# Performance work log

Measured on AMD Instinct MI355X. Metric: run time of the kernel, lower is better.

The kernel has to match this reference:

```python
import jax, jax.numpy as jnp
import numpy as np

B, N, F, NF = 4, 256, 256, 192
BN_EPS = 1e-5
NEG_SLOPE = 0.01  # torch F.leaky_relu default


def setup_inputs() -> dict:
    key = jax.random.key(0)
    ks = jax.random.split(key, 6)
    x = jax.random.normal(ks[0], (B, N, F), dtype=jnp.float32)
    # W_id is the identity adjacency broadcast to [B, N, N, 1]
    W_id = jnp.broadcast_to(jnp.eye(N, dtype=jnp.float32)[None, :, :, None], (B, N, N, 1))
    # conv2d_1: 1x1 conv, weight [nf, F, 1, 1] -> store as [F, nf]
    w1 = jax.random.normal(ks[1], (F, NF), dtype=jnp.float32) / np.sqrt(F)
    b1 = jax.random.normal(ks[2], (NF,), dtype=jnp.float32) * 0.01
    gamma = jnp.ones((NF,), dtype=jnp.float32)
    beta = jnp.zeros((NF,), dtype=jnp.float32)
    # conv2d_last: 1x1 conv nf -> 1
    w2 = jax.random.normal(ks[3], (NF,), dtype=jnp.float32) / np.sqrt(NF)
    b2 = jax.random.normal(ks[4], (), dtype=jnp.float32) * 0.01
    return {"x": x, "W_id": W_id, "w1": w1, "b1": b1, "gamma": gamma,
            "beta": beta, "w2": w2, "b2": b2}


def reference(x, W_id, w1, b1, gamma, beta, w2, b2):
    # pairwise abs diff: [B, N, N, F]
    diff = jnp.abs(x[:, :, None, :] - x[:, None, :, :])
    # 1x1 conv == channel matmul
    h = jnp.einsum('bijf,fc->bijc', diff, w1) + b1
    # BatchNorm2d, training mode: stats over (batch, i, j) per channel
    mean = jnp.mean(h, axis=(0, 1, 2))
    var = jnp.var(h, axis=(0, 1, 2))
    h = (h - mean) * jax.lax.rsqrt(var + BN_EPS) * gamma + beta
    h = jnp.where(h >= 0, h, NEG_SLOPE * h)  # leaky_relu
    # 1x1 conv nf -> 1: scores [B, N, N]
    s = jnp.einsum('bijc,c->bij', h, w2) + b2
    eye = W_id[..., 0]
    s = s - eye * 1e8  # mask self-edges
    A = jax.nn.softmax(s, axis=2)  # softmax over neighbors j
    # laplace operator: W_id - W_new, then squeeze -> [B, N, N]
    return eye - A
```

## Files before the change

kernel.cpp:

```cpp
#include <hip/hip_runtime.h>
#include <hip/hip_bf16.h>
#include <math.h>

#define BB 4
#define NN 256
#define FF 256
#define NF 192
#define MTOT 262144.0f
#define NB2 2560

typedef unsigned short u16;
typedef unsigned int   u32;
typedef __attribute__((ext_vector_type(8))) short bf16x8;
typedef __attribute__((ext_vector_type(4))) float f32x4;

#define W1P_OFF 0
#define AD_OFF  98304
#define P_OFF   99840

__device__ __forceinline__ u32 pk2(float a, float b) {
    u32 r;
    asm("v_cvt_pk_bf16_f32 %0, %1, %2" : "=v"(r) : "v"(a), "v"(b));
    return r;
}

__device__ __forceinline__ u16 f2bf(float f) {
    u32 u = __float_as_uint(f);
    return (u16)((u + 0x7FFFu + ((u >> 16) & 1u)) >> 16);
}

__global__ void k0_pack_w1(const float* __restrict__ w1, u16* __restrict__ w1p) {
    int idx = blockIdx.x * 256 + threadIdx.x;
    int e  = idx & 7;
    int c  = (idx >> 3) % NF;
    int fc = idx / (NF * 8);
    w1p[idx] = f2bf(w1[(fc * 8 + e) * NF + c]);
}

__device__ __forceinline__ void block_map(int bid, int& b, int& i, int& qj) {
    b = bid / 640;
    int r = bid % 640;
    int q, rr;
    if      (r < 256) { q = 0; rr = r; }
    else if (r < 448) { q = 1; rr = r - 256; }
    else if (r < 576) { q = 2; rr = r - 448; }
    else              { q = 3; rr = r - 576; }
    const int per = 4 - q;
    i  = q * 64 + rr / per;
    qj = q + rr % per;
}

__device__ __forceinline__ void gemm_core(const float* __restrict__ x,
        const u16* __restrict__ w1p, int b, int i, int qj, int t,
        float* sxi, uint4* sd, f32x4 acc[2][6]) {
    const int l = t & 63, l15 = l & 15, lg = l >> 4, w = t >> 6;
    const int jw = (w >> 1) * 32;
    const int cw = (w & 1) * 96;
    const int jrow = t >> 2;
    const int c0 = (t & 3) * 2;
    const int jglob = qj * 64 + jrow;
    const float* xpt = x + (size_t)(b * NN + jglob) * FF + c0 * 8;
    const int w0 = jrow * 8 + ((c0)     ^ (jrow & 7));
    const int w1i = jrow * 8 + ((c0 + 1) ^ (jrow & 7));
    int aidx[2][2];
    #pragma unroll
    for (int a = 0; a < 2; a++) {
        const int row = jw + a * 16 + l15;
        #pragma unroll
        for (int ks = 0; ks < 2; ks++)
            aidx[ks][a] = row * 8 + ((ks * 4 + lg) ^ (row & 7));
    }
    const int bbase = lg * NF + cw + l15;
    const bf16x8* w1p8 = (const bf16x8*)w1p;

    sxi[t] = x[(size_t)(b * NN + i) * FF + t];
    float4 xa0 = *(const float4*)(xpt);
    float4 xa1 = *(const float4*)(xpt + 4);
    float4 xb0 = *(const float4*)(xpt + 8);
    float4 xb1 = *(const float4*)(xpt + 12);
    bf16x8 bcur[6];
    #pragma unroll
    for (int n = 0; n < 6; n++) bcur[n] = w1p8[bbase + n * 16];
    __syncthreads();
    {
        const float* sx = sxi + c0 * 8;
        uint4 v0, v1;
        v0.x = pk2(fabsf(xa0.x - sx[0]),  fabsf(xa0.y - sx[1]));
        v0.y = pk2(fabsf(xa0.z - sx[2]),  fabsf(xa0.w - sx[3]));
        v0.z = pk2(fabsf(xa1.x - sx[4]),  fabsf(xa1.y - sx[5]));
        v0.w = pk2(fabsf(xa1.z - sx[6]),  fabsf(xa1.w - sx[7]));
        v1.x = pk2(fabsf(xb0.x - sx[8]),  fabsf(xb0.y - sx[9]));
        v1.y = pk2(fabsf(xb0.z - sx[10]), fabsf(xb0.w - sx[11]));
        v1.z = pk2(fabsf(xb1.x - sx[12]), fabsf(xb1.y - sx[13]));
        v1.w = pk2(fabsf(xb1.z - sx[14]), fabsf(xb1.w - sx[15]));
        sd[w0] = v0; sd[w1i] = v1;
    }

    #pragma unroll
    for (int a = 0; a < 2; a++)
        #pragma unroll
        for (int n = 0; n < 6; n++) acc[a][n] = (f32x4){0.f, 0.f, 0.f, 0.f};

    for (int kk = 0; kk < 4; ++kk) {
        __syncthreads();
        if (kk < 3) {
            const float* xp = xpt + (kk + 1) * 64;
            xa0 = *(const float4*)(xp);
            xa1 = *(const float4*)(xp + 4);
            xb0 = *(const float4*)(xp + 8);
            xb1 = *(const float4*)(xp + 12);
        }
        const int rb = (kk & 1) * 512;
        bf16x8 af[2][2];
        #pragma unroll
        for (int ks = 0; ks < 2; ks++)
            #pragma unroll
            for (int a = 0; a < 2; a++)
                af[ks][a] = *(const bf16x8*)&sd[rb + aidx[ks][a]];
        #pragma unroll
        for (int ks = 0; ks < 2; ks++) {
            const int s = kk * 2 + ks;
            #pragma unroll
            for (int n = 0; n < 6; n++) {
                acc[0][n] = __builtin_amdgcn_mfma_f32_16x16x32_bf16(af[ks][0], bcur[n], acc[0][n], 0, 0, 0);
                acc[1][n] = __builtin_amdgcn_mfma_f32_16x16x32_bf16(af[ks][1], bcur[n], acc[1][n], 0, 0, 0);
                if (s < 7)
                    bcur[n] = w1p8[(s + 1) * 768 + bbase + n * 16];
            }
        }
        if (kk < 3) {
            const int wb = ((kk + 1) & 1) * 512;
            const float* sx = sxi + (kk + 1) * 64 + c0 * 8;
            uint4 v0, v1;
            v0.x = pk2(fabsf(xa0.x - sx[0]),  fabsf(xa0.y - sx[1]));
            v0.y = pk2(fabsf(xa0.z - sx[2]),  fabsf(xa0.w - sx[3]));
            v0.z = pk2(fabsf(xa1.x - sx[4]),  fabsf(xa1.y - sx[5]));
            v0.w = pk2(fabsf(xa1.z - sx[6]),  fabsf(xa1.w - sx[7]));
            v1.x = pk2(fabsf(xb0.x - sx[8]),  fabsf(xb0.y - sx[9]));
            v1.y = pk2(fabsf(xb0.z - sx[10]), fabsf(xb0.w - sx[11]));
            v1.z = pk2(fabsf(xb1.x - sx[12]), fabsf(xb1.y - sx[13]));
            v1.w = pk2(fabsf(xb1.z - sx[14]), fabsf(xb1.w - sx[15]));
            sd[wb + w0] = v0; sd[wb + w1i] = v1;
        }
    }
}

__global__ __launch_bounds__(256, 4) void k1a_stats_gemm(
    const float* __restrict__ x, const u16* __restrict__ w1p,
    float* __restrict__ partials) {

    __shared__ float sxi[FF];
    __shared__ uint4 sd[2 * 512];
    __shared__ float sstat[4][96][2];

    int b, i, qj;
    block_map(blockIdx.x, b, i, qj);
    const int t = threadIdx.x;
    const int l = t & 63, l15 = l & 15, w = t >> 6;

    f32x4 acc[2][6];
    gemm_core(x, w1p, b, i, qj, t, sxi, sd, acc);

    float ps[6], pq[6];
    #pragma unroll
    for (int n = 0; n < 6; n++) {
        float s = 0.f, q = 0.f;
        #pragma unroll
        for (int a = 0; a < 2; a++) {
            const f32x4 v = acc[a][n];
            s += v.x + v.y + v.z + v.w;
            q += v.x * v.x + v.y * v.y + v.z * v.z + v.w * v.w;
        }
        s += __shfl_xor(s, 16); s += __shfl_xor(s, 32);
        q += __shfl_xor(q, 16); q += __shfl_xor(q, 32);
        ps[n] = s; pq[n] = q;
    }
    if (l < 16) {
        #pragma unroll
        for (int n = 0; n < 6; n++) {
            sstat[w][n * 16 + l15][0] = ps[n];
            sstat[w][n * 16 + l15][1] = pq[n];
        }
    }
    __syncthreads();
    if (t < NF) {
        const int ch = t / 96, cl = t % 96;
        float S = sstat[ch][cl][0] + sstat[ch + 2][cl][0];
        float Q = sstat[ch][cl][1] + sstat[ch + 2][cl][1];
        const float W = (qj > (i >> 6)) ? 2.0f : 1.0f;
        partials[(size_t)t * NB2 + blockIdx.x]        = S * W;
        partials[(size_t)(NF + t) * NB2 + blockIdx.x] = Q * W;
    }
}

__global__ void k2_stats(const float* __restrict__ partials,
                         const float* __restrict__ gamma, const float* __restrict__ beta,
                         float2* __restrict__ ad) {
    __shared__ float red[4][2];
    const int c = blockIdx.x;
    const int t = threadIdx.x;
    float S = 0.f, Q = 0.f;
    #pragma unroll
    for (int r = 0; r < 10; ++r) {
        const int blk = t + r * 256;
        S += partials[(size_t)c * NB2 + blk];
        Q += partials[(size_t)(NF + c) * NB2 + blk];
    }
    #pragma unroll
    for (int off = 1; off < 64; off <<= 1) { S += __shfl_xor(S, off); Q += __shfl_xor(Q, off); }
    if ((t & 63) == 0) { red[t >> 6][0] = S; red[t >> 6][1] = Q; }
    __syncthreads();
    if (t == 0) {
        S = red[0][0] + red[1][0] + red[2][0] + red[3][0];
        Q = red[0][1] + red[1][1] + red[2][1] + red[3][1];
        const float mean = S / MTOT;
        const float var  = Q / MTOT - mean * mean;
        const float rs   = 1.0f / sqrtf(var + 1e-5f);
        const float A = gamma[c] * rs;
        const float D = beta[c] - mean * A;
        ad[c] = make_float2(A, D);
    }
}

__global__ __launch_bounds__(256, 4) void k1b_score_gemm(
    const float* __restrict__ x, const u16* __restrict__ w1p,
    const float2* __restrict__ ad, const float* __restrict__ w2,
    float* __restrict__ out) {

    __shared__ float sxi[FF];
    __shared__ uint4 sd[2 * 512];
    __shared__ float sA[NF], sD[NF], sW2[NF];
    __shared__ float sS[2][64];

    int b, i, qj;
    block_map(blockIdx.x, b, i, qj);
    const int t = threadIdx.x;
    const int l = t & 63, l15 = l & 15, lg = l >> 4, w = t >> 6;
    const int jw = (w >> 1) * 32, cw = (w & 1) * 96;

    if (t < NF) {
        const float2 v = ad[t];
        sA[t] = v.x; sD[t] = v.y; sW2[t] = w2[t];
    }

    f32x4 acc[2][6];
    gemm_core(x, w1p, b, i, qj, t, sxi, sd, acc);

    float sj[2][4];
    #pragma unroll
    for (int a = 0; a < 2; a++)
        #pragma unroll
        for (int r = 0; r < 4; r++) sj[a][r] = 0.f;
    #pragma unroll
    for (int n = 0; n < 6; n++) {
        const int c = cw + n * 16 + l15;
        const float A = sA[c], D = sD[c], W = sW2[c];
        #pragma unroll
        for (int a = 0; a < 2; a++) {
            const f32x4 v = acc[a][n];
            float z;
            z = fmaf(v.x, A, D); sj[a][0] += fmaxf(z, 0.01f * z) * W;
            z = fmaf(v.y, A, D); sj[a][1] += fmaxf(z, 0.01f * z) * W;
            z = fmaf(v.z, A, D); sj[a][2] += fmaxf(z, 0.01f * z) * W;
            z = fmaf(v.w, A, D); sj[a][3] += fmaxf(z, 0.01f * z) * W;
        }
    }
    #pragma unroll
    for (int a = 0; a < 2; a++)
        #pragma unroll
        for (int r = 0; r < 4; r++) {
            float v = sj[a][r];
            v += __shfl_xor(v, 1); v += __shfl_xor(v, 2);
            v += __shfl_xor(v, 4); v += __shfl_xor(v, 8);
            if (l15 == 0) sS[w & 1][jw + a * 16 + (lg << 2) + r] = v;
        }
    __syncthreads();

    if (t < 64) {
        const float s = sS[0][t] + sS[1][t];
        const int jglob = qj * 64 + t;
        out[(size_t)(b * NN + i) * NN + jglob] = s;
        if (qj > (i >> 6))
            out[(size_t)(b * NN + jglob) * NN + i] = s;
    }
}

__global__ __launch_bounds__(256) void k3_softmax(float* __restrict__ out) {
    __shared__ float redA[4], redB[4];
    const int r = blockIdx.x, t = threadIdx.x, i = r & 255;
    float s = out[(size_t)r * NN + t];
    if (t == i) s -= 1e8f;
    float m = s;
    #pragma unroll
    for (int off = 1; off < 64; off <<= 1) m = fmaxf(m, __shfl_xor(m, off));
    if ((t & 63) == 0) redA[t >> 6] = m;
    __syncthreads();
    m = fmaxf(fmaxf(redA[0], redA[1]), fmaxf(redA[2], redA[3]));
    const float e = expf(s - m);
    float q = e;
    #pragma unroll
    for (int off = 1; off < 64; off <<= 1) q += __shfl_xor(q, off);
    if ((t & 63) == 0) redB[t >> 6] = q;
    __syncthreads();
    const float inv = 1.0f / (redB[0] + redB[1] + redB[2] + redB[3]);
    out[(size_t)r * NN + t] = (t == i ? 1.0f : 0.0f) - e * inv;
}

extern "C" void kernel_launch(void* const* d_in, const int* in_sizes, int n_in,
                              void* d_out, int out_size, void* d_ws, size_t ws_size,
                              hipStream_t stream) {
    const float* x     = (const float*)d_in[0];
    const float* w1    = (const float*)d_in[2];
    const float* gamma = (const float*)d_in[4];
    const float* beta  = (const float*)d_in[5];
    const float* w2    = (const float*)d_in[6];

    char* ws = (char*)d_ws;
    u16*    w1p      = (u16*)(ws + W1P_OFF);
    float2* ad       = (float2*)(ws + AD_OFF);
    float*  partials = (float*)(ws + P_OFF);
    float*  out      = (float*)d_out;

    k0_pack_w1    <<<dim3(192),  dim3(256), 0, stream>>>(w1, w1p);
    k1a_stats_gemm<<<dim3(NB2),  dim3(256), 0, stream>>>(x, w1p, partials);
    k2_stats      <<<dim3(NF),   dim3(256), 0, stream>>>(partials, gamma, beta, ad);
    k1b_score_gemm<<<dim3(NB2),  dim3(256), 0, stream>>>(x, w1p, ad, w2, out);
    k3_softmax    <<<dim3(BB*NN), dim3(256), 0, stream>>>(out);
}
```

Baseline: 134.2 us.

## Shrink GEMM tiles to 32 j-rows with 128-thread blocks and padded x_i smem

```diff
diff --git a/kernel.cpp b/kernel.cpp
--- a/kernel.cpp
+++ b/kernel.cpp
@@ -7,7 +7,7 @@
 #define FF 256
 #define NF 192
 #define MTOT 262144.0f
-#define NB2 2560
+#define NB32 4608
 
 typedef unsigned short u16;
 typedef unsigned int   u32;
@@ -17,6 +17,8 @@
 #define W1P_OFF 0
 #define AD_OFF  98304
 #define P_OFF   99840
+
+#define SXP(f) ((f) + (((f) >> 4) << 2))
 
 __device__ __forceinline__ u32 pk2(float a, float b) {
     u32 r;
@@ -38,34 +40,33 @@
 }
 
 __device__ __forceinline__ void block_map(int bid, int& b, int& i, int& qj) {
-    b = bid / 640;
-    int r = bid % 640;
-    int q, rr;
-    if      (r < 256) { q = 0; rr = r; }
-    else if (r < 448) { q = 1; rr = r - 256; }
-    else if (r < 576) { q = 2; rr = r - 448; }
-    else              { q = 3; rr = r - 576; }
-    const int per = 4 - q;
-    i  = q * 64 + rr / per;
-    qj = q + rr % per;
+    b = bid / 1152;
+    int r = bid % 1152;
+    int q = 0;
+    #pragma unroll
+    for (int k = 0; k < 7; ++k) {
+        const int seg = 32 * (8 - q);
+        if (r >= seg) { r -= seg; q++; }
+    }
+    const int per = 8 - q;
+    i  = q * 32 + r / per;
+    qj = q + r % per;
 }
 
 __device__ __forceinline__ void gemm_core(const float* __restrict__ x,
         const u16* __restrict__ w1p, int b, int i, int qj, int t,
         float* sxi, uint4* sd, f32x4 acc[2][6]) {
     const int l = t & 63, l15 = l & 15, lg = l >> 4, w = t >> 6;
-    const int jw = (w >> 1) * 32;
-    const int cw = (w & 1) * 96;
+    const int cw = w * 96;
     const int jrow = t >> 2;
     const int c0 = (t & 3) * 2;
-    const int jglob = qj * 64 + jrow;
-    const float* xpt = x + (size_t)(b * NN + jglob) * FF + c0 * 8;
-    const int w0 = jrow * 8 + ((c0)     ^ (jrow & 7));
+    const float* xpt = x + (size_t)(b * NN + qj * 32 + jrow) * FF + c0 * 8;
+    const int w0  = jrow * 8 + ((c0)     ^ (jrow & 7));
     const int w1i = jrow * 8 + ((c0 + 1) ^ (jrow & 7));
     int aidx[2][2];
     #pragma unroll
     for (int a = 0; a < 2; a++) {
-        const int row = jw + a * 16 + l15;
+        const int row = a * 16 + l15;
         #pragma unroll
         for (int ks = 0; ks < 2; ks++)
             aidx[ks][a] = row * 8 + ((ks * 4 + lg) ^ (row & 7));
@@ -73,7 +74,11 @@
     const int bbase = lg * NF + cw + l15;
     const bf16x8* w1p8 = (const bf16x8*)w1p;
 
-    sxi[t] = x[(size_t)(b * NN + i) * FF + t];
+    {
+        const float* xi = x + (size_t)(b * NN + i) * FF;
+        sxi[SXP(t)]       = xi[t];
+        sxi[SXP(t + 128)] = xi[t + 128];
+    }
     float4 xa0 = *(const float4*)(xpt);
     float4 xa1 = *(const float4*)(xpt + 4);
     float4 xb0 = *(const float4*)(xpt + 8);
@@ -83,7 +88,7 @@
     for (int n = 0; n < 6; n++) bcur[n] = w1p8[bbase + n * 16];
     __syncthreads();
     {
-        const float* sx = sxi + c0 * 8;
+        const float* sx = sxi + SXP(c0 * 8);
         uint4 v0, v1;
         v0.x = pk2(fabsf(xa0.x - sx[0]),  fabsf(xa0.y - sx[1]));
         v0.y = pk2(fabsf(xa0.z - sx[2]),  fabsf(xa0.w - sx[3]));
@@ -110,7 +115,7 @@
             xb0 = *(const float4*)(xp + 8);
             xb1 = *(const float4*)(xp + 12);
         }
-        const int rb = (kk & 1) * 512;
+        const int rb = (kk & 1) * 256;
         bf16x8 af[2][2];
         #pragma unroll
         for (int ks = 0; ks < 2; ks++)
@@ -129,8 +134,8 @@
             }
         }
         if (kk < 3) {
-            const int wb = ((kk + 1) & 1) * 512;
-            const float* sx = sxi + (kk + 1) * 64 + c0 * 8;
+            const int wb = ((kk + 1) & 1) * 256;
+            const float* sx = sxi + SXP((kk + 1) * 64 + c0 * 8);
             uint4 v0, v1;
             v0.x = pk2(fabsf(xa0.x - sx[0]),  fabsf(xa0.y - sx[1]));
             v0.y = pk2(fabsf(xa0.z - sx[2]),  fabsf(xa0.w - sx[3]));
@@ -145,23 +150,23 @@
     }
 }
 
-__global__ __launch_bounds__(256, 4) void k1a_stats_gemm(
+__global__ __launch_bounds__(128, 4) void k1a_stats_gemm(
     const float* __restrict__ x, const u16* __restrict__ w1p,
     float* __restrict__ partials) {
 
-    __shared__ float sxi[FF];
-    __shared__ uint4 sd[2 * 512];
-    __shared__ float sstat[4][96][2];
+    __shared__ float sxi[320];
+    __shared__ uint4 sd[2 * 256];
 
     int b, i, qj;
     block_map(blockIdx.x, b, i, qj);
     const int t = threadIdx.x;
     const int l = t & 63, l15 = l & 15, w = t >> 6;
+    const int cw = w * 96;
 
     f32x4 acc[2][6];
     gemm_core(x, w1p, b, i, qj, t, sxi, sd, acc);
 
-    float ps[6], pq[6];
+    const float W = (qj > (i >> 5)) ? 2.0f : 1.0f;
     #pragma unroll
     for (int n = 0; n < 6; n++) {
         float s = 0.f, q = 0.f;
@@ -173,23 +178,11 @@
         }
         s += __shfl_xor(s, 16); s += __shfl_xor(s, 32);
         q += __shfl_xor(q, 16); q += __shfl_xor(q, 32);
-        ps[n] = s; pq[n] = q;
-    }
-    if (l < 16) {
-        #pragma unroll
-        for (int n = 0; n < 6; n++) {
-            sstat[w][n * 16 + l15][0] = ps[n];
-            sstat[w][n * 16 + l15][1] = pq[n];
-        }
-    }
-    __syncthreads();
-    if (t < NF) {
-        const int ch = t / 96, cl = t % 96;
-        float S = sstat[ch][cl][0] + sstat[ch + 2][cl][0];
-        float Q = sstat[ch][cl][1] + sstat[ch + 2][cl][1];
-        const float W = (qj > (i >> 6)) ? 2.0f : 1.0f;
-        partials[(size_t)t * NB2 + blockIdx.x]        = S * W;
-        partials[(size_t)(NF + t) * NB2 + blockIdx.x] = Q * W;
+        if (l < 16) {
+            const int c = cw + n * 16 + l;
+            partials[(size_t)c * NB32 + blockIdx.x]        = s * W;
+            partials[(size_t)(NF + c) * NB32 + blockIdx.x] = q * W;
+        }
     }
 }
 
@@ -201,10 +194,10 @@
     const int t = threadIdx.x;
     float S = 0.f, Q = 0.f;
     #pragma unroll
-    for (int r = 0; r < 10; ++r) {
+    for (int r = 0; r < 18; ++r) {
         const int blk = t + r * 256;
-        S += partials[(size_t)c * NB2 + blk];
-        Q += partials[(size_t)(NF + c) * NB2 + blk];
+        S += partials[(size_t)c * NB32 + blk];
+        Q += partials[(size_t)(NF + c) * NB32 + blk];
     }
     #pragma unroll
     for (int off = 1; off < 64; off <<= 1) { S += __shfl_xor(S, off); Q += __shfl_xor(Q, off); }
@@ -222,25 +215,25 @@
     }
 }
 
-__global__ __launch_bounds__(256, 4) void k1b_score_gemm(
+__global__ __launch_bounds__(128, 4) void k1b_score_gemm(
     const float* __restrict__ x, const u16* __restrict__ w1p,
     const float2* __restrict__ ad, const float* __restrict__ w2,
     float* __restrict__ out) {
 
-    __shared__ float sxi[FF];
-    __shared__ uint4 sd[2 * 512];
+    __shared__ float sxi[320];
+    __shared__ uint4 sd[2 * 256];
     __shared__ float sA[NF], sD[NF], sW2[NF];
-    __shared__ float sS[2][64];
+    __shared__ float sS[2][32];
 
     int b, i, qj;
     block_map(blockIdx.x, b, i, qj);
     const int t = threadIdx.x;
     const int l = t & 63, l15 = l & 15, lg = l >> 4, w = t >> 6;
-    const int jw = (w >> 1) * 32, cw = (w & 1) * 96;
-
-    if (t < NF) {
-        const float2 v = ad[t];
-        sA[t] = v.x; sD[t] = v.y; sW2[t] = w2[t];
+    const int cw = w * 96;
+
+    for (int c = t; c < NF; c += 128) {
+        const float2 v = ad[c];
+        sA[c] = v.x; sD[c] = v.y; sW2[c] = w2[c];
     }
 
     f32x4 acc[2][6];
@@ -272,15 +265,15 @@
             float v = sj[a][r];
             v += __shfl_xor(v, 1); v += __shfl_xor(v, 2);
             v += __shfl_xor(v, 4); v += __shfl_xor(v, 8);
-            if (l15 == 0) sS[w & 1][jw + a * 16 + (lg << 2) + r] = v;
-        }
-    __syncthreads();
-
-    if (t < 64) {
+            if (l15 == 0) sS[w][a * 16 + (lg << 2) + r] = v;
+        }
+    __syncthreads();
+
+    if (t < 32) {
         const float s = sS[0][t] + sS[1][t];
-        const int jglob = qj * 64 + t;
+        const int jglob = qj * 32 + t;
         out[(size_t)(b * NN + i) * NN + jglob] = s;
-        if (qj > (i >> 6))
+        if (qj > (i >> 5))
             out[(size_t)(b * NN + jglob) * NN + i] = s;
     }
 }
@@ -321,9 +314,9 @@
     float*  partials = (float*)(ws + P_OFF);
     float*  out      = (float*)d_out;
 
-    k0_pack_w1    <<<dim3(192),  dim3(256), 0, stream>>>(w1, w1p);
-    k1a_stats_gemm<<<dim3(NB2),  dim3(256), 0, stream>>>(x, w1p, partials);
-    k2_stats      <<<dim3(NF),   dim3(256), 0, stream>>>(partials, gamma, beta, ad);
-    k1b_score_gemm<<<dim3(NB2),  dim3(256), 0, stream>>>(x, w1p, ad, w2, out);
+    k0_pack_w1    <<<dim3(192),   dim3(256), 0, stream>>>(w1, w1p);
+    k1a_stats_gemm<<<dim3(NB32),  dim3(128), 0, stream>>>(x, w1p, partials);
+    k2_stats      <<<dim3(NF),    dim3(256), 0, stream>>>(partials, gamma, beta, ad);
+    k1b_score_gemm<<<dim3(NB32),  dim3(128), 0, stream>>>(x, w1p, ad, w2, out);
     k3_softmax    <<<dim3(BB*NN), dim3(256), 0, stream>>>(out);
 }
```

New measurement: 136.0 us. About the same (+1.3%).
